# Kernel tuning notes

Hardware: AMD Instinct MI355X
Metric: run time of the kernel (lower is better)

The kernel has to match this reference:

```python
import jax, jax.numpy as jnp
import numpy as np

B, IN, H = 4096, 1024, 1024


def setup_inputs() -> dict:
    key = jax.random.key(0)
    ks = jax.random.split(key, 20)
    s_in = 1.0 / np.sqrt(IN)
    s_h = 1.0 / np.sqrt(H)
    def lin(kw, kb, fan_in, scale):
        W = jax.random.uniform(kw, (H, fan_in), jnp.float32, -scale, scale)
        b = jax.random.uniform(kb, (H,), jnp.float32, -scale, scale)
        return W, b
    Wxf, bxf = lin(ks[0], ks[1], IN, s_in)
    Whf, bhf = lin(ks[2], ks[3], H, s_h)
    Wxi, bxi = lin(ks[4], ks[5], IN, s_in)
    Whi, bhi = lin(ks[6], ks[7], H, s_h)
    Wxo, bxo = lin(ks[8], ks[9], IN, s_in)
    Who, bho = lin(ks[10], ks[11], H, s_h)
    Wxc, bxc = lin(ks[12], ks[13], IN, s_in)
    Whc, bhc = lin(ks[14], ks[15], H, s_h)
    x = jax.random.normal(ks[16], (B, IN), jnp.float32)
    c = jax.random.normal(ks[17], (B, H), jnp.float32)
    h = jax.random.normal(ks[18], (B, H), jnp.float32)
    return dict(x=x, c=c, h=h,
                Wxf=Wxf, bxf=bxf, Whf=Whf, bhf=bhf,
                Wxi=Wxi, bxi=bxi, Whi=Whi, bhi=bhi,
                Wxo=Wxo, bxo=bxo, Who=Who, bho=bho,
                Wxc=Wxc, bxc=bxc, Whc=Whc, bhc=bhc)


def reference(x, c, h,
              Wxf, bxf, Whf, bhf,
              Wxi, bxi, Whi, bhi,
              Wxo, bxo, Who, bho,
              Wxc, bxc, Whc, bhc):
    # Fuse the 8 small GEMMs into two batched GEMMs: x @ Wx^T and h @ Wh^T
    # with gate outputs concatenated along the hidden dim [f, i, o, c~].
    Wx = jnp.concatenate([Wxf, Wxi, Wxo, Wxc], axis=0)   # [4H, IN]
    Wh = jnp.concatenate([Whf, Whi, Who, Whc], axis=0)   # [4H, H]
    bx = jnp.concatenate([bxf, bxi, bxo, bxc], axis=0)   # [4H]
    bh = jnp.concatenate([bhf, bhi, bho, bhc], axis=0)   # [4H]
    gates = x @ Wx.T + h @ Wh.T + (bx + bh)              # [B, 4H]
    hs = Wxf.shape[0]
    f = jax.nn.sigmoid(gates[:, 0 * hs:1 * hs])
    i = jax.nn.sigmoid(gates[:, 1 * hs:2 * hs])
    o = jax.nn.sigmoid(gates[:, 2 * hs:3 * hs])
    ctil = jnp.tanh(gates[:, 3 * hs:4 * hs])
    ct = f * c + ctil * i
    ht = jnp.tanh(ct) * o
    return (ct, ht)
```

## Files before the change

### kernel.cpp

```cpp
#include <hip/hip_runtime.h>
#include <hip/hip_bf16.h>
#include <stdint.h>

typedef __hip_bfloat16 bf16;
typedef __attribute__((ext_vector_type(8))) short short8;
typedef __attribute__((ext_vector_type(16))) float floatx16;

#define AS1(p) ((const __attribute__((address_space(1))) void*)(p))
#define AS3(p) ((__attribute__((address_space(3))) void*)(p))

#define M_DIM 4096
#define H_DIM 1024
#define STAGE 24576

__device__ __forceinline__ unsigned short f2bf(float f) {
    uint32_t u = __float_as_uint(f);
    uint32_t r = (u + 0x7FFFu + ((u >> 16) & 1u)) >> 16;
    return (unsigned short)r;
}
__device__ __forceinline__ float fast_sigmoid(float v) {
    return 1.0f / (1.0f + __expf(-v));
}
__device__ __forceinline__ float fast_tanh(float v) {
    return 2.0f / (1.0f + __expf(-2.0f * v)) - 1.0f;
}

__global__ __launch_bounds__(256)
void pack_bf16(const float* __restrict__ x, const float* __restrict__ h,
               const float* Wxf, const float* Wxi, const float* Wxo, const float* Wxc,
               const float* Whf, const float* Whi, const float* Who, const float* Whc,
               unsigned short* __restrict__ ws)
{
    const int w = threadIdx.x >> 6;
    const int l = threadIdx.x & 63;
    const uint32_t W = blockIdx.x * 4u + (uint32_t)w;

    const uint32_t r  = (uint32_t)l & 31u;
    const uint32_t kh = (uint32_t)l >> 5;

    const float* src;
    uint32_t row, kq;
    if (W < 16384u) {
        const uint32_t ch4 = W & 3u;
        kq = (W >> 2) & 127u;
        const uint32_t mx = W >> 9;
        src = (kq < 64u) ? x : h;
        row = mx * 128u + ch4 * 32u + r;
    } else {
        const uint32_t V  = W - 16384u;
        kq = V & 127u;
        const uint32_t U  = V >> 7;
        const uint32_t b8 = U & 7u;
        const uint32_t ny = U >> 3;
        const uint32_t g  = b8 >> 1;
        const uint32_t nh = b8 & 1u;
        if (kq < 64u)
            src = (g == 0) ? Wxf : (g == 1) ? Wxi : (g == 2) ? Wxo : Wxc;
        else
            src = (g == 0) ? Whf : (g == 1) ? Whi : (g == 2) ? Who : Whc;
        row = ny * 64u + nh * 32u + r;
    }
    const float* s = src + (size_t)row * 1024u + (kq & 63u) * 16u + kh * 8u;
    const float4 v0 = *(const float4*)s;
    const float4 v1 = *(const float4*)(s + 4);
    short8 pk;
    pk[0] = (short)f2bf(v0.x); pk[1] = (short)f2bf(v0.y);
    pk[2] = (short)f2bf(v0.z); pk[3] = (short)f2bf(v0.w);
    pk[4] = (short)f2bf(v1.x); pk[5] = (short)f2bf(v1.y);
    pk[6] = (short)f2bf(v1.z); pk[7] = (short)f2bf(v1.w);
    *(short8*)(ws + (size_t)W * 512u + (uint32_t)l * 8u) = pk;
}

#define GLL(srcp, dstp) __builtin_amdgcn_global_load_lds(AS1(srcp), AS3(dstp), 16, 0, 0)
#define WAITB(N) do {                                                         \
    asm volatile("s_waitcnt vmcnt(" #N ") lgkmcnt(0)\ns_barrier" ::: "memory");\
    __builtin_amdgcn_sched_barrier(0);                                        \
} while (0)

#define MFMA32(a, b, c) __builtin_amdgcn_mfma_f32_32x32x16_bf16((a), (b), (c), 0, 0, 0)

#define ISSUE(SL) do {                                                        \
    GLL(p0, lds + (SL)*STAGE + loff0); p0 += ks0;                             \
    GLL(p1, lds + (SL)*STAGE + loff1); p1 += ks1;                             \
    GLL(p2, lds + (SL)*STAGE + loff2); p2 += ks2;                             \
} while (0)

#define COMPUTE(SC) do {                                                      \
    short8 a_  = *(const short8*)(ldsA + (SC)*STAGE + 0);                     \
    short8 b0_ = *(const short8*)(ldsB + (SC)*STAGE + 0);                     \
    short8 b1_ = *(const short8*)(ldsB + (SC)*STAGE + 2048);                  \
    short8 b2_ = *(const short8*)(ldsB + (SC)*STAGE + 4096);                  \
    short8 b3_ = *(const short8*)(ldsB + (SC)*STAGE + 6144);                  \
    acc0 = MFMA32(a_, b0_, acc0);                                             \
    acc1 = MFMA32(a_, b1_, acc1);                                             \
    acc2 = MFMA32(a_, b2_, acc2);                                             \
    acc3 = MFMA32(a_, b3_, acc3);                                             \
    a_  = *(const short8*)(ldsA + (SC)*STAGE + 4096);                         \
    b0_ = *(const short8*)(ldsB + (SC)*STAGE + 8192);                         \
    b1_ = *(const short8*)(ldsB + (SC)*STAGE + 8192 + 2048);                  \
    b2_ = *(const short8*)(ldsB + (SC)*STAGE + 8192 + 4096);                  \
    b3_ = *(const short8*)(ldsB + (SC)*STAGE + 8192 + 6144);                  \
    acc0 = MFMA32(a_, b0_, acc0);                                             \
    acc1 = MFMA32(a_, b1_, acc1);                                             \
    acc2 = MFMA32(a_, b2_, acc2);                                             \
    acc3 = MFMA32(a_, b3_, acc3);                                             \
} while (0)

#define ITER(SC, SL) do { WAITB(3); ISSUE(SL); COMPUTE(SC); } while (0)

__global__ __launch_bounds__(512, 4)
void lstm_fused_kernel(const unsigned short* __restrict__ ws,
                       const float* __restrict__ c,
                       const float* __restrict__ bxf, const float* __restrict__ bhf,
                       const float* __restrict__ bxi, const float* __restrict__ bhi,
                       const float* __restrict__ bxo, const float* __restrict__ bho,
                       const float* __restrict__ bxc, const float* __restrict__ bhc,
                       float* __restrict__ out)
{
    __shared__ __align__(16) char lds[3 * STAGE];

    const int tid  = threadIdx.x;
    const int w    = tid >> 6;
    const int lane = tid & 63;

    const int bid = blockIdx.x;
    const int mx  = bid >> 4;
    const int ny  = ((bid & 7) << 1) | ((bid >> 3) & 1);
    const int bm0 = mx * 128;
    const int bn0 = ny * 64;

    const int wM2 = w >> 1;
    const int wN  = w & 1;

    const unsigned short* p0; const unsigned short* p1; const unsigned short* p2;
    uint32_t loff0, loff1, loff2, ks0, ks1, ks2;
#define CHDEC(CH, P, LO, KS) do {                                             \
    const int ch_ = (CH);                                                     \
    if (ch_ < 8) {                                                            \
        const uint32_t kc_ = (uint32_t)ch_ >> 2, c4_ = (uint32_t)ch_ & 3u;    \
        P = ws + ((uint32_t)mx * 512u + kc_ * 4u + c4_) * 512u                \
               + (uint32_t)lane * 8u;                                         \
        KS = 4096u;                                                           \
    } else {                                                                  \
        const uint32_t b_ = (uint32_t)(ch_ - 8), kc_ = b_ >> 3, b8_ = b_ & 7u;\
        P = ws + (16384u + ((uint32_t)ny * 8u + b8_) * 128u + kc_) * 512u     \
               + (uint32_t)lane * 8u;                                         \
        KS = 1024u;                                                           \
    }                                                                         \
    LO = (uint32_t)ch_ * 1024u;                                               \
} while (0)
    CHDEC(w * 3 + 0, p0, loff0, ks0);
    CHDEC(w * 3 + 1, p1, loff1, ks1);
    CHDEC(w * 3 + 2, p2, loff2, ks2);
#undef CHDEC

    const char* ldsA = lds + (uint32_t)lane * 16u + (uint32_t)wM2 * 1024u;
    const char* ldsB = lds + (uint32_t)lane * 16u + 8192u + (uint32_t)wN * 1024u;

    floatx16 acc0 = {0}, acc1 = {0}, acc2 = {0}, acc3 = {0};

    ISSUE(0);
    ISSUE(1);

    for (int t = 0; t < 20; ++t) {
        ITER(0, 2); ITER(1, 0); ITER(2, 1);
    }
    ITER(0, 2);
    ITER(1, 0);
    WAITB(3); COMPUTE(2);
    WAITB(0); COMPUTE(0);

    const int colg = bn0 + wN * 32 + (lane & 31);
    const int lq   = lane >> 5;
    const int row0 = bm0 + wM2 * 32;
    float* out_ct = out;
    float* out_ht = out + (size_t)M_DIM * H_DIM;

    const float bf_ = bxf[colg] + bhf[colg];
    const float bi_ = bxi[colg] + bhi[colg];
    const float bo_ = bxo[colg] + bho[colg];
    const float bc_ = bxc[colg] + bhc[colg];

#pragma unroll
    for (int r = 0; r < 16; ++r) {
        const int ri  = (r & 3) + 8 * (r >> 2) + 4 * lq;
        const int row = row0 + ri;
        const float f    = fast_sigmoid(acc0[r] + bf_);
        const float ii   = fast_sigmoid(acc1[r] + bi_);
        const float o    = fast_sigmoid(acc2[r] + bo_);
        const float ctil = fast_tanh(acc3[r] + bc_);
        const float cv   = c[(size_t)row * H_DIM + colg];
        const float ctn  = f * cv + ctil * ii;
        const float htn  = fast_tanh(ctn) * o;
        out_ct[(size_t)row * H_DIM + colg] = ctn;
        out_ht[(size_t)row * H_DIM + colg] = htn;
    }
}

extern "C" void kernel_launch(void* const* d_in, const int* in_sizes, int n_in,
                              void* d_out, int out_size, void* d_ws, size_t ws_size,
                              hipStream_t stream) {
    (void)in_sizes; (void)n_in; (void)out_size; (void)ws_size;
    const float* x   = (const float*)d_in[0];
    const float* c   = (const float*)d_in[1];
    const float* h   = (const float*)d_in[2];
    const float* Wxf = (const float*)d_in[3];  const float* bxf = (const float*)d_in[4];
    const float* Whf = (const float*)d_in[5];  const float* bhf = (const float*)d_in[6];
    const float* Wxi = (const float*)d_in[7];  const float* bxi = (const float*)d_in[8];
    const float* Whi = (const float*)d_in[9];  const float* bhi = (const float*)d_in[10];
    const float* Wxo = (const float*)d_in[11]; const float* bxo = (const float*)d_in[12];
    const float* Who = (const float*)d_in[13]; const float* bho = (const float*)d_in[14];
    const float* Wxc = (const float*)d_in[15]; const float* bxc = (const float*)d_in[16];
    const float* Whc = (const float*)d_in[17]; const float* bhc = (const float*)d_in[18];
    float* out = (float*)d_out;
    unsigned short* ws = (unsigned short*)d_ws;

    pack_bf16<<<8192, 256, 0, stream>>>(x, h,
        Wxf, Wxi, Wxo, Wxc, Whf, Whi, Who, Whc, ws);

    lstm_fused_kernel<<<512, 512, 0, stream>>>(ws, c,
        bxf, bhf, bxi, bhi, bxo, bho, bxc, bhc, out);
}
```

Before: 228.3 us.

## Switch GEMM to 16x16x32 MFMA with register-loaded B and smaller LDS tiles

Reworks the fused LSTM GEMM to use 16x16x32 bf16 MFMA over 128x32 output tiles with 256-thread blocks. Only the activation (A) tile is staged through LDS via global_load_lds. Each wave loads its weight (B) fragments straight into registers, double-buffered across iterations. The pack kernel layout and the block-to-tile swizzle are changed to match. The aim is to cut LDS traffic and footprint and raise block count and occupancy, at the cost of more global weight loads per block and more, smaller MFMAs.

```diff
diff --git a/kernel.cpp b/kernel.cpp
--- a/kernel.cpp
+++ b/kernel.cpp
@@ -4,14 +4,13 @@
 
 typedef __hip_bfloat16 bf16;
 typedef __attribute__((ext_vector_type(8))) short short8;
-typedef __attribute__((ext_vector_type(16))) float floatx16;
+typedef __attribute__((ext_vector_type(4))) float floatx4;
 
 #define AS1(p) ((const __attribute__((address_space(1))) void*)(p))
 #define AS3(p) ((__attribute__((address_space(3))) void*)(p))
 
 #define M_DIM 4096
 #define H_DIM 1024
-#define STAGE 24576
 
 __device__ __forceinline__ unsigned short f2bf(float f) {
     uint32_t u = __float_as_uint(f);
@@ -35,32 +34,32 @@
     const int l = threadIdx.x & 63;
     const uint32_t W = blockIdx.x * 4u + (uint32_t)w;
 
-    const uint32_t r  = (uint32_t)l & 31u;
-    const uint32_t kh = (uint32_t)l >> 5;
+    const uint32_t kg = (uint32_t)l >> 4;
+    const uint32_t rr = (uint32_t)l & 15u;
 
     const float* src;
-    uint32_t row, kq;
+    uint32_t row, ktl;
     if (W < 16384u) {
-        const uint32_t ch4 = W & 3u;
-        kq = (W >> 2) & 127u;
+        const uint32_t ch = W & 7u;
+        const uint32_t KT = (W >> 3) & 63u;
         const uint32_t mx = W >> 9;
-        src = (kq < 64u) ? x : h;
-        row = mx * 128u + ch4 * 32u + r;
+        src = (KT < 32u) ? x : h;
+        ktl = KT & 31u;
+        row = mx * 128u + ch * 16u + rr;
     } else {
         const uint32_t V  = W - 16384u;
-        kq = V & 127u;
-        const uint32_t U  = V >> 7;
-        const uint32_t b8 = U & 7u;
-        const uint32_t ny = U >> 3;
-        const uint32_t g  = b8 >> 1;
-        const uint32_t nh = b8 & 1u;
-        if (kq < 64u)
+        const uint32_t g  = V & 3u;
+        const uint32_t KT = (V >> 2) & 63u;
+        const uint32_t cc = (V >> 8) & 1u;
+        const uint32_t ny = V >> 9;
+        if (KT < 32u)
             src = (g == 0) ? Wxf : (g == 1) ? Wxi : (g == 2) ? Wxo : Wxc;
         else
             src = (g == 0) ? Whf : (g == 1) ? Whi : (g == 2) ? Who : Whc;
-        row = ny * 64u + nh * 32u + r;
+        ktl = KT & 31u;
+        row = ny * 32u + cc * 16u + rr;
     }
-    const float* s = src + (size_t)row * 1024u + (kq & 63u) * 16u + kh * 8u;
+    const float* s = src + (size_t)row * 1024u + ktl * 32u + kg * 8u;
     const float4 v0 = *(const float4*)s;
     const float4 v1 = *(const float4*)(s + 4);
     short8 pk;
@@ -72,43 +71,58 @@
 }
 
 #define GLL(srcp, dstp) __builtin_amdgcn_global_load_lds(AS1(srcp), AS3(dstp), 16, 0, 0)
-#define WAITB(N) do {                                                         \
+#define WAITB(N) do {                                                          \
     asm volatile("s_waitcnt vmcnt(" #N ") lgkmcnt(0)\ns_barrier" ::: "memory");\
-    __builtin_amdgcn_sched_barrier(0);                                        \
-} while (0)
-
-#define MFMA32(a, b, c) __builtin_amdgcn_mfma_f32_32x32x16_bf16((a), (b), (c), 0, 0, 0)
-
-#define ISSUE(SL) do {                                                        \
-    GLL(p0, lds + (SL)*STAGE + loff0); p0 += ks0;                             \
-    GLL(p1, lds + (SL)*STAGE + loff1); p1 += ks1;                             \
-    GLL(p2, lds + (SL)*STAGE + loff2); p2 += ks2;                             \
-} while (0)
-
-#define COMPUTE(SC) do {                                                      \
-    short8 a_  = *(const short8*)(ldsA + (SC)*STAGE + 0);                     \
-    short8 b0_ = *(const short8*)(ldsB + (SC)*STAGE + 0);                     \
-    short8 b1_ = *(const short8*)(ldsB + (SC)*STAGE + 2048);                  \
-    short8 b2_ = *(const short8*)(ldsB + (SC)*STAGE + 4096);                  \
-    short8 b3_ = *(const short8*)(ldsB + (SC)*STAGE + 6144);                  \
-    acc0 = MFMA32(a_, b0_, acc0);                                             \
-    acc1 = MFMA32(a_, b1_, acc1);                                             \
-    acc2 = MFMA32(a_, b2_, acc2);                                             \
-    acc3 = MFMA32(a_, b3_, acc3);                                             \
-    a_  = *(const short8*)(ldsA + (SC)*STAGE + 4096);                         \
-    b0_ = *(const short8*)(ldsB + (SC)*STAGE + 8192);                         \
-    b1_ = *(const short8*)(ldsB + (SC)*STAGE + 8192 + 2048);                  \
-    b2_ = *(const short8*)(ldsB + (SC)*STAGE + 8192 + 4096);                  \
-    b3_ = *(const short8*)(ldsB + (SC)*STAGE + 8192 + 6144);                  \
-    acc0 = MFMA32(a_, b0_, acc0);                                             \
-    acc1 = MFMA32(a_, b1_, acc1);                                             \
-    acc2 = MFMA32(a_, b2_, acc2);                                             \
-    acc3 = MFMA32(a_, b3_, acc3);                                             \
-} while (0)
-
-#define ITER(SC, SL) do { WAITB(3); ISSUE(SL); COMPUTE(SC); } while (0)
-
-__global__ __launch_bounds__(512, 4)
+    __builtin_amdgcn_sched_barrier(0);                                         \
+} while (0)
+
+#define MFMA16(a, b, c) __builtin_amdgcn_mfma_f32_16x16x32_bf16((a), (b), (c), 0, 0, 0)
+
+#define ISSUE_A(SL) do {                                                       \
+    GLL(pA0, lds + (SL)*8192 + loffA);                                         \
+    GLL(pA1, lds + (SL)*8192 + loffA + 1024);                                  \
+    pA0 += 4096; pA1 += 4096;                                                  \
+} while (0)
+
+#define ISSUE_B(BB) do {                                                       \
+    bb##BB##0 = *(const short8*)(pB);                                          \
+    bb##BB##1 = *(const short8*)(pB + 512);                                    \
+    bb##BB##2 = *(const short8*)(pB + 1024);                                   \
+    bb##BB##3 = *(const short8*)(pB + 1536);                                   \
+    pB += 2048;                                                                \
+} while (0)
+
+#define COMPUTE(SC, BB) do {                                                   \
+    const short8 a0_ = *(const short8*)(ldsA + (SC)*8192 + 0);                 \
+    const short8 a1_ = *(const short8*)(ldsA + (SC)*8192 + 1024);              \
+    const short8 a2_ = *(const short8*)(ldsA + (SC)*8192 + 2048);              \
+    const short8 a3_ = *(const short8*)(ldsA + (SC)*8192 + 3072);              \
+    acc[0][0] = MFMA16(a0_, bb##BB##0, acc[0][0]);                             \
+    acc[0][1] = MFMA16(a1_, bb##BB##0, acc[0][1]);                             \
+    acc[0][2] = MFMA16(a2_, bb##BB##0, acc[0][2]);                             \
+    acc[0][3] = MFMA16(a3_, bb##BB##0, acc[0][3]);                             \
+    acc[1][0] = MFMA16(a0_, bb##BB##1, acc[1][0]);                             \
+    acc[1][1] = MFMA16(a1_, bb##BB##1, acc[1][1]);                             \
+    acc[1][2] = MFMA16(a2_, bb##BB##1, acc[1][2]);                             \
+    acc[1][3] = MFMA16(a3_, bb##BB##1, acc[1][3]);                             \
+    acc[2][0] = MFMA16(a0_, bb##BB##2, acc[2][0]);                             \
+    acc[2][1] = MFMA16(a1_, bb##BB##2, acc[2][1]);                             \
+    acc[2][2] = MFMA16(a2_, bb##BB##2, acc[2][2]);                             \
+    acc[2][3] = MFMA16(a3_, bb##BB##2, acc[2][3]);                             \
+    acc[3][0] = MFMA16(a0_, bb##BB##3, acc[3][0]);                             \
+    acc[3][1] = MFMA16(a1_, bb##BB##3, acc[3][1]);                             \
+    acc[3][2] = MFMA16(a2_, bb##BB##3, acc[3][2]);                             \
+    acc[3][3] = MFMA16(a3_, bb##BB##3, acc[3][3]);                             \
+} while (0)
+
+#define ITER(SC, SL, CUR, NXT) do {                                            \
+    WAITB(2);                                                                  \
+    ISSUE_B(NXT);                                                              \
+    ISSUE_A(SL);                                                               \
+    COMPUTE(SC, CUR);                                                          \
+} while (0)
+
+__global__ __launch_bounds__(256, 2)
 void lstm_fused_kernel(const unsigned short* __restrict__ ws,
                        const float* __restrict__ c,
                        const float* __restrict__ bxf, const float* __restrict__ bhf,
@@ -117,62 +131,64 @@
                        const float* __restrict__ bxc, const float* __restrict__ bhc,
                        float* __restrict__ out)
 {
-    __shared__ __align__(16) char lds[3 * STAGE];
+    __shared__ __align__(16) char lds[3 * 8192];
 
     const int tid  = threadIdx.x;
     const int w    = tid >> 6;
     const int lane = tid & 63;
 
-    const int bid = blockIdx.x;
-    const int mx  = bid >> 4;
-    const int ny  = ((bid & 7) << 1) | ((bid >> 3) & 1);
+    const int bid  = blockIdx.x;
+    const int wgid = (bid & 7) * 128 + (bid >> 3);
+    const int ny  = wgid >> 5;
+    const int mx  = wgid & 31;
     const int bm0 = mx * 128;
-    const int bn0 = ny * 64;
-
-    const int wM2 = w >> 1;
-    const int wN  = w & 1;
-
-    const unsigned short* p0; const unsigned short* p1; const unsigned short* p2;
-    uint32_t loff0, loff1, loff2, ks0, ks1, ks2;
-#define CHDEC(CH, P, LO, KS) do {                                             \
-    const int ch_ = (CH);                                                     \
-    if (ch_ < 8) {                                                            \
-        const uint32_t kc_ = (uint32_t)ch_ >> 2, c4_ = (uint32_t)ch_ & 3u;    \
-        P = ws + ((uint32_t)mx * 512u + kc_ * 4u + c4_) * 512u                \
-               + (uint32_t)lane * 8u;                                         \
-        KS = 4096u;                                                           \
-    } else {                                                                  \
-        const uint32_t b_ = (uint32_t)(ch_ - 8), kc_ = b_ >> 3, b8_ = b_ & 7u;\
-        P = ws + (16384u + ((uint32_t)ny * 8u + b8_) * 128u + kc_) * 512u     \
-               + (uint32_t)lane * 8u;                                         \
-        KS = 1024u;                                                           \
-    }                                                                         \
-    LO = (uint32_t)ch_ * 1024u;                                               \
-} while (0)
-    CHDEC(w * 3 + 0, p0, loff0, ks0);
-    CHDEC(w * 3 + 1, p1, loff1, ks1);
-    CHDEC(w * 3 + 2, p2, loff2, ks2);
-#undef CHDEC
-
-    const char* ldsA = lds + (uint32_t)lane * 16u + (uint32_t)wM2 * 1024u;
-    const char* ldsB = lds + (uint32_t)lane * 16u + 8192u + (uint32_t)wN * 1024u;
-
-    floatx16 acc0 = {0}, acc1 = {0}, acc2 = {0}, acc3 = {0};
-
-    ISSUE(0);
-    ISSUE(1);
-
-    for (int t = 0; t < 20; ++t) {
-        ITER(0, 2); ITER(1, 0); ITER(2, 1);
+    const int bn0 = ny * 32;
+
+    const int wM = w >> 1;
+    const int wN = w & 1;
+
+    const unsigned short* pA0 = ws + ((uint32_t)mx * 512u + (uint32_t)w * 2u) * 512u
+                                   + (uint32_t)lane * 8u;
+    const unsigned short* pA1 = pA0 + 512u;
+    const uint32_t loffA = (uint32_t)w * 2048u;
+
+    const unsigned short* pB = ws + 8388608u
+                                  + ((uint32_t)(ny * 2 + wN)) * 131072u
+                                  + (uint32_t)lane * 8u;
+
+    const char* ldsA = lds + (uint32_t)wM * 4096u + (uint32_t)lane * 16u;
+
+    short8 bb00, bb01, bb02, bb03;
+    short8 bb10, bb11, bb12, bb13;
+
+    floatx4 acc[4][4];
+#pragma unroll
+    for (int g = 0; g < 4; ++g)
+#pragma unroll
+        for (int mt = 0; mt < 4; ++mt)
+            acc[g][mt] = (floatx4){0.f, 0.f, 0.f, 0.f};
+
+    ISSUE_A(0);
+    ISSUE_B(0);
+    ISSUE_A(1);
+
+    for (int t = 0; t < 10; ++t) {
+        ITER(0, 2, 0, 1);
+        ITER(1, 0, 1, 0);
+        ITER(2, 1, 0, 1);
+        ITER(0, 2, 1, 0);
+        ITER(1, 0, 0, 1);
+        ITER(2, 1, 1, 0);
     }
-    ITER(0, 2);
-    ITER(1, 0);
-    WAITB(3); COMPUTE(2);
-    WAITB(0); COMPUTE(0);
-
-    const int colg = bn0 + wN * 32 + (lane & 31);
-    const int lq   = lane >> 5;
-    const int row0 = bm0 + wM2 * 32;
+    ITER(0, 2, 0, 1);
+    ITER(1, 0, 1, 0);
+    WAITB(2); ISSUE_B(1); COMPUTE(2, 0);
+    WAITB(0); COMPUTE(0, 1);
+
+    const int lrc   = lane & 15;
+    const int lquad = lane >> 4;
+    const int colg  = bn0 + wN * 16 + lrc;
+    const int wrow  = wM * 64;
     float* out_ct = out;
     float* out_ht = out + (size_t)M_DIM * H_DIM;
 
@@ -182,18 +198,20 @@
     const float bc_ = bxc[colg] + bhc[colg];
 
 #pragma unroll
-    for (int r = 0; r < 16; ++r) {
-        const int ri  = (r & 3) + 8 * (r >> 2) + 4 * lq;
-        const int row = row0 + ri;
-        const float f    = fast_sigmoid(acc0[r] + bf_);
-        const float ii   = fast_sigmoid(acc1[r] + bi_);
-        const float o    = fast_sigmoid(acc2[r] + bo_);
-        const float ctil = fast_tanh(acc3[r] + bc_);
-        const float cv   = c[(size_t)row * H_DIM + colg];
-        const float ctn  = f * cv + ctil * ii;
-        const float htn  = fast_tanh(ctn) * o;
-        out_ct[(size_t)row * H_DIM + colg] = ctn;
-        out_ht[(size_t)row * H_DIM + colg] = htn;
+    for (int mt = 0; mt < 4; ++mt) {
+#pragma unroll
+        for (int r = 0; r < 4; ++r) {
+            const int row = bm0 + wrow + mt * 16 + lquad * 4 + r;
+            const float f    = fast_sigmoid(acc[0][mt][r] + bf_);
+            const float ii   = fast_sigmoid(acc[1][mt][r] + bi_);
+            const float o    = fast_sigmoid(acc[2][mt][r] + bo_);
+            const float ctil = fast_tanh(acc[3][mt][r] + bc_);
+            const float cv   = c[(size_t)row * H_DIM + colg];
+            const float ctn  = f * cv + ctil * ii;
+            const float htn  = fast_tanh(ctn) * o;
+            out_ct[(size_t)row * H_DIM + colg] = ctn;
+            out_ht[(size_t)row * H_DIM + colg] = htn;
+        }
     }
 }
 
@@ -218,6 +236,6 @@
     pack_bf16<<<8192, 256, 0, stream>>>(x, h,
         Wxf, Wxi, Wxo, Wxc, Whf, Whi, Who, Whc, ws);
 
-    lstm_fused_kernel<<<512, 512, 0, stream>>>(ws, c,
+    lstm_fused_kernel<<<1024, 256, 0, stream>>>(ws, c,
         bxf, bhf, bxi, bhi, bxo, bho, bxc, bhc, out);
 }
```

Result: slower. 245.6 us (+7.6%).
